# Kernel optimization log

Hardware: AMD Instinct MI355X
Metric: run time of the kernel (lower is better)

## Reference

```python
import jax, jax.numpy as jnp
from jax import lax
import numpy as np

B, T, N, F_IN, H, E, K = 8, 32, 500, 64, 128, 8000, 3
LN_EPS = 1e-5


def setup_inputs() -> dict:
    key = jax.random.key(0)
    ks = jax.random.split(key, 10)
    x = jax.random.normal(ks[0], (B, T, N, F_IN), dtype=jnp.float32)
    edge_index = jax.random.randint(ks[1], (2, E), 0, N, dtype=jnp.int64)
    edge_weight = jax.random.uniform(ks[2], (E,), dtype=jnp.float32)
    # GCNConv: linear (in->out) + bias
    W_gcn = jax.random.normal(ks[3], (F_IN, H), dtype=jnp.float32) / np.sqrt(F_IN)
    b_gcn = jnp.zeros((H,), dtype=jnp.float32)
    # Conv1d(H, H, K): weight (O, I, K)
    W_temp = jax.random.normal(ks[4], (H, H, K), dtype=jnp.float32) / np.sqrt(H * K)
    b_temp = jnp.zeros((H,), dtype=jnp.float32)
    # LayerNorm(H)
    ln_w = jnp.ones((H,), dtype=jnp.float32)
    ln_b = jnp.zeros((H,), dtype=jnp.float32)
    # residual Linear (in->out)
    W_res = jax.random.normal(ks[5], (F_IN, H), dtype=jnp.float32) / np.sqrt(F_IN)
    b_res = jnp.zeros((H,), dtype=jnp.float32)
    return {"x": x, "edge_index": edge_index, "edge_weight": edge_weight,
            "W_gcn": W_gcn, "b_gcn": b_gcn, "W_temp": W_temp, "b_temp": b_temp,
            "ln_w": ln_w, "ln_b": ln_b, "W_res": W_res, "b_res": b_res}


def reference(x, edge_index, edge_weight, W_gcn, b_gcn, W_temp, b_temp, ln_w, ln_b, W_res, b_res):
    Bv, Tv, Nv, Fv = x.shape
    Hv = W_gcn.shape[1]
    res = x @ W_res + b_res  # (B,T,N,H)

    # ---- spatial GCNConv on B*T replicated graphs (vectorized, no index offsetting) ----
    xf = x.reshape(Bv * Tv, Nv, Fv) @ W_gcn  # (BT,N,H)
    src, dst = edge_index[0], edge_index[1]
    loops = jnp.arange(Nv, dtype=edge_index.dtype)
    src2 = jnp.concatenate([src, loops])
    dst2 = jnp.concatenate([dst, loops])
    ew2 = jnp.concatenate([edge_weight, jnp.ones((Nv,), dtype=edge_weight.dtype)])
    deg = jax.ops.segment_sum(ew2, dst2, num_segments=Nv)
    dinv = jnp.where(deg > 0, deg ** -0.5, 0.0)
    norm = dinv[src2] * ew2 * dinv[dst2]  # (E+N,)
    msgs = xf[:, src2, :] * norm[None, :, None]  # (BT, E+N, H)
    agg = jax.vmap(lambda m: jax.ops.segment_sum(m, dst2, num_segments=Nv))(msgs)
    h = jax.nn.gelu(agg + b_gcn, approximate=False)  # (BT,N,H)

    # ---- temporal Conv1d over T ----
    h = h.reshape(Bv, Tv, Nv, Hv).transpose(0, 2, 3, 1).reshape(Bv * Nv, Hv, Tv)
    pad = K // 2
    h = lax.conv_general_dilated(h, W_temp, window_strides=(1,), padding=[(pad, pad)],
                                 dimension_numbers=("NCH", "OIH", "NCH"))
    h = jax.nn.gelu(h + b_temp[None, :, None], approximate=False)
    h = h.reshape(Bv, Nv, Hv, Tv).transpose(0, 3, 1, 2)  # (B,T,N,H)

    # ---- fused residual + LayerNorm over last dim ----
    y = h + res
    mu = jnp.mean(y, axis=-1, keepdims=True)
    var = jnp.mean((y - mu) ** 2, axis=-1, keepdims=True)
    return (y - mu) * lax.rsqrt(var + LN_EPS) * ln_w + ln_b
```

## Files before the change

### kernel.cpp

```cpp
#include <hip/hip_runtime.h>
#include <hip/hip_bf16.h>
#include <math.h>

#define Bv 8
#define Tv 32
#define Nv 500
#define NP 512
#define Fin 64
#define Hv 128
#define Ev 8000
#define Kv 3
#define BT (Bv*Tv)
#define ROWS (BT*Nv)
#define NCOL (BT*Fin)
#define TP (Tv+2)
#define KK (Kv*Hv)
#define LDSROW 144

typedef __attribute__((ext_vector_type(8))) short s8v;
typedef __attribute__((ext_vector_type(4))) float f4v;

__device__ __forceinline__ float gelu_exact(float v){
    float t  = v*0.70710678118654752440f;
    float ax = fabsf(t);
    float k  = __builtin_amdgcn_rcpf(fmaf(0.3275911f, ax, 1.0f));
    float p  = k*fmaf(k, fmaf(k, fmaf(k, fmaf(k, 1.061405429f, -1.453152027f),
                                      1.421413741f), -0.284496736f), 0.254829592f);
    float e  = __expf(-ax*ax);
    float er = fmaf(-p, e, 1.0f);
    er = copysignf(er, t);
    return 0.5f*v*(1.0f + er);
}
__device__ __forceinline__ short f2bs(float f){
    union { __hip_bfloat16 h; short s; } u;
    u.h = __float2bfloat16(f);
    return u.s;
}
__device__ __forceinline__ float b2f(short s){
    union { unsigned int i; float f; } u;
    u.i = ((unsigned int)(unsigned short)s) << 16;
    return u.f;
}

__global__ __launch_bounds__(1024) void k_prep0(const float* __restrict__ x,
        short* __restrict__ X2b, short* __restrict__ XT,
        float* __restrict__ Af32,
        const float* __restrict__ W, const float* __restrict__ Wg,
        const float* __restrict__ Wr,
        short* __restrict__ W2, short* __restrict__ Wgt, short* __restrict__ Wrt,
        const int* __restrict__ ei, const float* __restrict__ ew,
        float* __restrict__ dinv){
    __shared__ float sdeg[Nv];
    int bid = blockIdx.x;
    int tid = threadIdx.x;
    if (bid == 0){
        if (tid < Nv) sdeg[tid] = 1.0f;
        __syncthreads();
        for (int e = tid; e < Ev; e += 1024)
            atomicAdd(&sdeg[ei[Ev + e]], ew[e]);
        __syncthreads();
        if (tid < Nv){
            float d = sdeg[tid];
            dinv[tid] = (d > 0.f) ? rsqrtf(d) : 0.f;
        }
    } else if (bid <= 64){
        int i = (bid-1)*1024 + tid;
        ((float4*)Af32)[i] = make_float4(0.f,0.f,0.f,0.f);
    } else if (bid <= 2064){
        int gid = (bid-65)*1024 + tid;
        int row = gid >> 4, c4 = gid & 15;
        int bt = row / Nv;
        int n  = row - bt*Nv;
        float4 v = ((const float4*)x)[gid];
        short4 sv;
        sv.x = f2bs(v.x); sv.y = f2bs(v.y); sv.z = f2bs(v.z); sv.w = f2bs(v.w);
        *(short4*)(X2b + (size_t)n*NCOL + bt*64 + c4*4) = sv;
        int colb = bt*64 + c4*4;
        XT[(size_t)(colb+0)*NP + n] = sv.x;
        XT[(size_t)(colb+1)*NP + n] = sv.y;
        XT[(size_t)(colb+2)*NP + n] = sv.z;
        XT[(size_t)(colb+3)*NP + n] = sv.w;
    } else if (bid <= 2112){
        int idx = (bid-2065)*1024 + tid;
        int col = idx/3, rem = idx - col*3;
        short4 z = {0,0,0,0};
        *(short4*)(XT + (size_t)col*NP + Nv + rem*4) = z;
    } else {
        int idx = (bid-2113)*1024 + tid;
        if (idx < Hv*Hv*Kv){
            int o = idx/(Hv*Kv);
            int rem = idx - o*(Hv*Kv);
            int i = rem/Kv, k = rem - i*Kv;
            W2[o*KK + k*Hv + i] = f2bs(W[idx]);
        } else if (idx < Hv*Hv*Kv + Hv*64){
            int j = idx - Hv*Hv*Kv;
            int o = j >> 6, k = j & 63;
            Wgt[j] = f2bs(Wg[k*Hv + o]);
        } else if (idx < Hv*Hv*Kv + 2*Hv*64){
            int j = idx - Hv*Hv*Kv - Hv*64;
            int o = j >> 6, k = j & 63;
            Wrt[j] = f2bs(Wr[k*Hv + o]);
        }
    }
}

__global__ __launch_bounds__(1024) void k_prep1(const int* __restrict__ ei,
        const float* __restrict__ ew, const float* __restrict__ dinv,
        float* __restrict__ Af32){
    int e = blockIdx.x*1024 + threadIdx.x;
    if (e < Ev){
        int s = ei[e], d = ei[Ev + e];
        atomicAdd(&Af32[(size_t)d*NP + s], dinv[s]*ew[e]*dinv[d]);
    }
    if (blockIdx.x == 0 && threadIdx.x < Nv){
        float dv = dinv[threadIdx.x];
        atomicAdd(&Af32[(size_t)threadIdx.x*NP + threadIdx.x], dv*dv);
    }
}

__global__ __launch_bounds__(1024) void k_cvt(const float* __restrict__ Af32,
        short* __restrict__ Ab){
    int i = blockIdx.x*1024 + threadIdx.x;
    float4 v = ((const float4*)Af32)[i];
    short4 s;
    s.x = f2bs(v.x); s.y = f2bs(v.y); s.z = f2bs(v.z); s.w = f2bs(v.w);
    ((short4*)Ab)[i] = s;
}

__global__ __launch_bounds__(256) void k_gemm(const short* __restrict__ Ab,
        const short* __restrict__ XT, short* __restrict__ AGG2){
    int tid  = threadIdx.x;
    int w    = tid >> 6;
    int lane = tid & 63;
    int quad = lane >> 4;
    int laneo = lane & 15;
    int bid = blockIdx.x;
    int jt = bid & 127, it = bid >> 7;
    int i0 = it*128;
    int j0 = jt*128 + w*32;

    f4v acc[8][2];
    #pragma unroll
    for (int m = 0; m < 8; ++m){
        acc[m][0] = (f4v){0.f,0.f,0.f,0.f};
        acc[m][1] = (f4v){0.f,0.f,0.f,0.f};
    }
    #pragma unroll 2
    for (int ks = 0; ks < 16; ++ks){
        int k0 = ks*32 + quad*8;
        s8v bfr[2];
        #pragma unroll
        for (int nt = 0; nt < 2; ++nt)
            bfr[nt] = *(const s8v*)(XT + (size_t)(j0 + nt*16 + laneo)*NP + k0);
        #pragma unroll
        for (int m = 0; m < 8; ++m){
            s8v afr = *(const s8v*)(Ab + (size_t)(i0 + m*16 + laneo)*NP + k0);
            acc[m][0] = __builtin_amdgcn_mfma_f32_16x16x32_bf16(afr, bfr[0], acc[m][0], 0,0,0);
            acc[m][1] = __builtin_amdgcn_mfma_f32_16x16x32_bf16(afr, bfr[1], acc[m][1], 0,0,0);
        }
    }
    #pragma unroll
    for (int m = 0; m < 8; ++m){
        #pragma unroll
        for (int r = 0; r < 4; ++r){
            int row = i0 + m*16 + quad*4 + r;
            if (row < Nv){
                #pragma unroll
                for (int nt = 0; nt < 2; ++nt)
                    AGG2[(size_t)row*NCOL + j0 + nt*16 + laneo] = f2bs(acc[m][nt][r]);
            }
        }
    }
}

__global__ __launch_bounds__(256, 2) void k_mega(
        const short* __restrict__ AGG2, const short* __restrict__ X2b,
        const short* __restrict__ W2, const short* __restrict__ Wgt,
        const short* __restrict__ Wrt,
        const float* __restrict__ bg, const float* __restrict__ btm,
        const float* __restrict__ br, const float* __restrict__ lw,
        const float* __restrict__ lb, float* __restrict__ out){
    __shared__ short hs[4*TP*LDSROW];
    __shared__ float red[Tv][4][2];
    int tid  = threadIdx.x;
    int w    = tid >> 6;
    int lane = tid & 63;
    int quad = lane >> 4;
    int laneo = lane & 15;
    int bid = blockIdx.x;
    int b  = bid / 125;
    int n0 = (bid - b*125) * 4;
    int o_base = w*32;

    float bgv[2], bbv[2], brv[2], lwv[2], lbv[2];
    #pragma unroll
    for (int nt = 0; nt < 2; ++nt){
        int o = o_base + nt*16 + laneo;
        bgv[nt] = bg[o]; bbv[nt] = btm[o]; brv[nt] = br[o];
        lwv[nt] = lw[o]; lbv[nt] = lb[o];
    }

    s8v bwg[2][2];
    #pragma unroll
    for (int nt = 0; nt < 2; ++nt){
        const short* wp = Wgt + (o_base + nt*16 + laneo)*64 + quad*8;
        bwg[nt][0] = *(const s8v*)wp;
        bwg[nt][1] = *(const s8v*)(wp + 32);
    }

    if (tid < 128){
        int node = tid >> 5, rem = tid & 31;
        int tp = (rem >> 4)*(TP-1), c8 = rem & 15;
        s8v z = {0,0,0,0,0,0,0,0};
        *(s8v*)&hs[node*(TP*LDSROW) + tp*LDSROW + c8*8] = z;
    }

    for (int g = 0; g < 4; ++g){
        int n = n0 + g;
        const short* ap = AGG2 + ((size_t)n*BT + b*Tv)*64;
        #pragma unroll
        for (int m = 0; m < 2; ++m){
            const short* arp = ap + (m*16 + laneo)*64 + quad*8;
            s8v a0 = *(const s8v*)arp;
            s8v a1 = *(const s8v*)(arp + 32);
            f4v h0 = {0.f,0.f,0.f,0.f}, h1 = {0.f,0.f,0.f,0.f};
            h0 = __builtin_amdgcn_mfma_f32_16x16x32_bf16(a0, bwg[0][0], h0, 0,0,0);
            h0 = __builtin_amdgcn_mfma_f32_16x16x32_bf16(a1, bwg[0][1], h0, 0,0,0);
            h1 = __builtin_amdgcn_mfma_f32_16x16x32_bf16(a0, bwg[1][0], h1, 0,0,0);
            h1 = __builtin_amdgcn_mfma_f32_16x16x32_bf16(a1, bwg[1][1], h1, 0,0,0);
            #pragma unroll
            for (int r = 0; r < 4; ++r){
                int tp = m*16 + quad*4 + r + 1;
                short* hrow = &hs[g*(TP*LDSROW) + tp*LDSROW];
                hrow[o_base + laneo]      = f2bs(gelu_exact(h0[r] + bgv[0]));
                hrow[o_base + 16 + laneo] = f2bs(gelu_exact(h1[r] + bgv[1]));
            }
        }
    }

    s8v breg[2][12], bwr[2][2];
    #pragma unroll
    for (int nt = 0; nt < 2; ++nt){
        int o = o_base + nt*16 + laneo;
        const short* wp = W2 + o*KK + quad*8;
        #pragma unroll
        for (int s = 0; s < 12; ++s)
            breg[nt][s] = *(const s8v*)(wp + s*32);
        const short* wr = Wrt + o*64 + quad*8;
        bwr[nt][0] = *(const s8v*)wr;
        bwr[nt][1] = *(const s8v*)(wr + 32);
    }
    __syncthreads();

    for (int g = 0; g < 4; ++g){
        int n = n0 + g;
        f4v acc[2][2];
        #pragma unroll
        for (int m = 0; m < 2; ++m)
            #pragma unroll
            for (int nt = 0; nt < 2; ++nt)
                acc[m][nt] = (f4v){0.f,0.f,0.f,0.f};
        #pragma unroll
        for (int m = 0; m < 2; ++m){
            #pragma unroll
            for (int s = 0; s < 12; ++s){
                int k  = s >> 2;
                int i0 = (s & 3) * 32;
                int tp = m*16 + laneo + k;
                s8v a = *(const s8v*)&hs[g*(TP*LDSROW) + tp*LDSROW + i0 + quad*8];
                acc[m][0] = __builtin_amdgcn_mfma_f32_16x16x32_bf16(a, breg[0][s], acc[m][0], 0,0,0);
                acc[m][1] = __builtin_amdgcn_mfma_f32_16x16x32_bf16(a, breg[1][s], acc[m][1], 0,0,0);
            }
        }
        f4v racc[2][2];
        #pragma unroll
        for (int m = 0; m < 2; ++m)
            #pragma unroll
            for (int nt = 0; nt < 2; ++nt)
                racc[m][nt] = (f4v){0.f,0.f,0.f,0.f};
        const short* xp = X2b + ((size_t)n*BT + b*Tv)*64;
        #pragma unroll
        for (int m = 0; m < 2; ++m){
            const short* xrp = xp + (m*16 + laneo)*64 + quad*8;
            s8v a0 = *(const s8v*)xrp;
            s8v a1 = *(const s8v*)(xrp + 32);
            racc[m][0] = __builtin_amdgcn_mfma_f32_16x16x32_bf16(a0, bwr[0][0], racc[m][0], 0,0,0);
            racc[m][0] = __builtin_amdgcn_mfma_f32_16x16x32_bf16(a1, bwr[0][1], racc[m][0], 0,0,0);
            racc[m][1] = __builtin_amdgcn_mfma_f32_16x16x32_bf16(a0, bwr[1][0], racc[m][1], 0,0,0);
            racc[m][1] = __builtin_amdgcn_mfma_f32_16x16x32_bf16(a1, bwr[1][1], racc[m][1], 0,0,0);
        }
        size_t obase = ((size_t)b*Tv*Nv + n)*Hv;
        float yv[2][2][4];
        float srow[2][4], ssrow[2][4];
        #pragma unroll
        for (int m = 0; m < 2; ++m)
            #pragma unroll
            for (int r = 0; r < 4; ++r){ srow[m][r] = 0.f; ssrow[m][r] = 0.f; }
        #pragma unroll
        for (int m = 0; m < 2; ++m){
            #pragma unroll
            for (int nt = 0; nt < 2; ++nt){
                #pragma unroll
                for (int r = 0; r < 4; ++r){
                    float gv = gelu_exact(acc[m][nt][r] + bbv[nt]);
                    float y = gv + racc[m][nt][r] + brv[nt];
                    yv[m][nt][r] = y;
                    srow[m][r] += y; ssrow[m][r] += y*y;
                }
            }
        }
        #pragma unroll
        for (int m = 0; m < 2; ++m)
            #pragma unroll
            for (int r = 0; r < 4; ++r){
                #pragma unroll
                for (int msk = 8; msk >= 1; msk >>= 1){
                    srow[m][r]  += __shfl_xor(srow[m][r],  msk, 64);
                    ssrow[m][r] += __shfl_xor(ssrow[m][r], msk, 64);
                }
            }
        if (laneo == 0){
            #pragma unroll
            for (int m = 0; m < 2; ++m)
                #pragma unroll
                for (int r = 0; r < 4; ++r){
                    int t = m*16 + quad*4 + r;
                    red[t][w][0] = srow[m][r];
                    red[t][w][1] = ssrow[m][r];
                }
        }
        __syncthreads();
        #pragma unroll
        for (int m = 0; m < 2; ++m){
            #pragma unroll
            for (int r = 0; r < 4; ++r){
                int t = m*16 + quad*4 + r;
                float s  = red[t][0][0] + red[t][1][0] + red[t][2][0] + red[t][3][0];
                float ss = red[t][0][1] + red[t][1][1] + red[t][2][1] + red[t][3][1];
                float mu = s * (1.f/128.f);
                float var = fmaxf(ss * (1.f/128.f) - mu*mu, 0.f);
                float rstd = rsqrtf(var + 1e-5f);
                #pragma unroll
                for (int nt = 0; nt < 2; ++nt){
                    int o = o_base + nt*16 + laneo;
                    out[obase + (size_t)t*Nv*Hv + o] =
                        (yv[m][nt][r] - mu)*rstd*lwv[nt] + lbv[nt];
                }
            }
        }
        __syncthreads();
    }
}

extern "C" void kernel_launch(void* const* d_in, const int* in_sizes, int n_in,
                              void* d_out, int out_size, void* d_ws, size_t ws_size,
                              hipStream_t stream){
    const float* x   = (const float*)d_in[0];
    const int*   ei  = (const int*)d_in[1];
    const float* ew  = (const float*)d_in[2];
    const float* Wg  = (const float*)d_in[3];
    const float* bg  = (const float*)d_in[4];
    const float* Wtm = (const float*)d_in[5];
    const float* btm = (const float*)d_in[6];
    const float* lw  = (const float*)d_in[7];
    const float* lb  = (const float*)d_in[8];
    const float* Wr  = (const float*)d_in[9];
    const float* br  = (const float*)d_in[10];
    float* out = (float*)d_out;

    char* ws = (char*)d_ws;
    float* dinv = (float*)(ws + 0);
    float* Af32 = (float*)(ws + 4096);
    short* Ab   = (short*)(ws + 1052672);
    short* W2   = (short*)(ws + 1576960);
    short* Wgt  = (short*)(ws + 1675264);
    short* Wrt  = (short*)(ws + 1691648);
    short* X2b  = (short*)(ws + 1708032);
    short* XT   = (short*)(ws + 18092032);
    short* AGG2 = (short*)(ws + 34869248);

    k_prep0<<<2177, 1024, 0, stream>>>(x, X2b, XT, Af32, Wtm, Wg, Wr,
                                       W2, Wgt, Wrt, ei, ew, dinv);
    k_prep1<<<8, 1024, 0, stream>>>(ei, ew, dinv, Af32);
    k_cvt  <<<64, 1024, 0, stream>>>(Af32, Ab);
    k_gemm <<<512, 256, 0, stream>>>(Ab, XT, AGG2);
    k_mega <<<(Bv*Nv)/4, 256, 0, stream>>>(AGG2, X2b, W2, Wgt, Wrt,
                                           bg, btm, br, lw, lb, out);
}
```

Measured before the change: 220.8 us.

## Transpose x via LDS tiles and drop the X2b bf16 copy

The prep kernel now builds the transposed bf16 XT buffer through a shared-memory tile transpose, so global stores are coalesced 16-byte vectors instead of scattered 2-byte writes, and it writes the zero padding inline. The separate node-major bf16 copy X2b is removed. The mega kernel instead reads fp32 x directly and converts it to bf16 in registers for the residual MFMA. This cuts a large write and its later read, at the cost of wider fp32 loads in the mega kernel.

Measured after the change: 220.9 us. About the same (+0.0%).

```diff
diff --git a/kernel.cpp b/kernel.cpp
--- a/kernel.cpp
+++ b/kernel.cpp
@@ -36,57 +36,63 @@
     u.h = __float2bfloat16(f);
     return u.s;
 }
-__device__ __forceinline__ float b2f(short s){
-    union { unsigned int i; float f; } u;
-    u.i = ((unsigned int)(unsigned short)s) << 16;
-    return u.f;
-}
-
-__global__ __launch_bounds__(1024) void k_prep0(const float* __restrict__ x,
-        short* __restrict__ X2b, short* __restrict__ XT,
-        float* __restrict__ Af32,
+
+__global__ __launch_bounds__(256) void k_t(const float* __restrict__ x,
+        short* __restrict__ XT, float* __restrict__ Af32,
         const float* __restrict__ W, const float* __restrict__ Wg,
         const float* __restrict__ Wr,
         short* __restrict__ W2, short* __restrict__ Wgt, short* __restrict__ Wrt,
         const int* __restrict__ ei, const float* __restrict__ ew,
         float* __restrict__ dinv){
-    __shared__ float sdeg[Nv];
     int bid = blockIdx.x;
     int tid = threadIdx.x;
-    if (bid == 0){
-        if (tid < Nv) sdeg[tid] = 1.0f;
+    if (bid < 2048){
+        __shared__ short t[64][72];
+        int bt = bid >> 3;
+        int n0 = (bid & 7) * 64;
+        int r   = tid >> 2;
+        int c16 = (tid & 3) * 16;
+        int n = n0 + r;
+        short sv[16];
+        if (n < Nv){
+            const float4* src = (const float4*)(x + ((size_t)bt*Nv + n)*64 + c16);
+            #pragma unroll
+            for (int j = 0; j < 4; ++j){
+                float4 v = src[j];
+                sv[j*4+0]=f2bs(v.x); sv[j*4+1]=f2bs(v.y);
+                sv[j*4+2]=f2bs(v.z); sv[j*4+3]=f2bs(v.w);
+            }
+        } else {
+            #pragma unroll
+            for (int j = 0; j < 16; ++j) sv[j] = 0;
+        }
+        #pragma unroll
+        for (int j = 0; j < 16; ++j) t[r][c16+j] = sv[j];
         __syncthreads();
-        for (int e = tid; e < Ev; e += 1024)
+        int cc  = tid >> 2;
+        int nn0 = (tid & 3) * 16;
+        short ov[16];
+        #pragma unroll
+        for (int j = 0; j < 16; ++j) ov[j] = t[nn0+j][cc];
+        short* dst = XT + (size_t)(bt*64 + cc)*NP + n0 + nn0;
+        *(s8v*)dst       = *(s8v*)&ov[0];
+        *(s8v*)(dst + 8) = *(s8v*)&ov[8];
+    } else if (bid == 2048){
+        __shared__ float sdeg[Nv];
+        for (int i = tid; i < Nv; i += 256) sdeg[i] = 1.0f;
+        __syncthreads();
+        for (int e = tid; e < Ev; e += 256)
             atomicAdd(&sdeg[ei[Ev + e]], ew[e]);
         __syncthreads();
-        if (tid < Nv){
-            float d = sdeg[tid];
-            dinv[tid] = (d > 0.f) ? rsqrtf(d) : 0.f;
-        }
-    } else if (bid <= 64){
-        int i = (bid-1)*1024 + tid;
+        for (int i = tid; i < Nv; i += 256){
+            float d = sdeg[i];
+            dinv[i] = (d > 0.f) ? rsqrtf(d) : 0.f;
+        }
+    } else if (bid <= 2304){
+        int i = (bid-2049)*256 + tid;
         ((float4*)Af32)[i] = make_float4(0.f,0.f,0.f,0.f);
-    } else if (bid <= 2064){
-        int gid = (bid-65)*1024 + tid;
-        int row = gid >> 4, c4 = gid & 15;
-        int bt = row / Nv;
-        int n  = row - bt*Nv;
-        float4 v = ((const float4*)x)[gid];
-        short4 sv;
-        sv.x = f2bs(v.x); sv.y = f2bs(v.y); sv.z = f2bs(v.z); sv.w = f2bs(v.w);
-        *(short4*)(X2b + (size_t)n*NCOL + bt*64 + c4*4) = sv;
-        int colb = bt*64 + c4*4;
-        XT[(size_t)(colb+0)*NP + n] = sv.x;
-        XT[(size_t)(colb+1)*NP + n] = sv.y;
-        XT[(size_t)(colb+2)*NP + n] = sv.z;
-        XT[(size_t)(colb+3)*NP + n] = sv.w;
-    } else if (bid <= 2112){
-        int idx = (bid-2065)*1024 + tid;
-        int col = idx/3, rem = idx - col*3;
-        short4 z = {0,0,0,0};
-        *(short4*)(XT + (size_t)col*NP + Nv + rem*4) = z;
     } else {
-        int idx = (bid-2113)*1024 + tid;
+        int idx = (bid-2305)*256 + tid;
         if (idx < Hv*Hv*Kv){
             int o = idx/(Hv*Kv);
             int rem = idx - o*(Hv*Kv);
@@ -104,7 +110,7 @@
     }
 }
 
-__global__ __launch_bounds__(1024) void k_prep1(const int* __restrict__ ei,
+__global__ __launch_bounds__(1024) void k_scat(const int* __restrict__ ei,
         const float* __restrict__ ew, const float* __restrict__ dinv,
         float* __restrict__ Af32){
     int e = blockIdx.x*1024 + threadIdx.x;
@@ -174,7 +180,7 @@
 }
 
 __global__ __launch_bounds__(256, 2) void k_mega(
-        const short* __restrict__ AGG2, const short* __restrict__ X2b,
+        const short* __restrict__ AGG2, const float* __restrict__ x,
         const short* __restrict__ W2, const short* __restrict__ Wgt,
         const short* __restrict__ Wrt,
         const float* __restrict__ bg, const float* __restrict__ btm,
@@ -278,12 +284,18 @@
             #pragma unroll
             for (int nt = 0; nt < 2; ++nt)
                 racc[m][nt] = (f4v){0.f,0.f,0.f,0.f};
-        const short* xp = X2b + ((size_t)n*BT + b*Tv)*64;
         #pragma unroll
         for (int m = 0; m < 2; ++m){
-            const short* xrp = xp + (m*16 + laneo)*64 + quad*8;
-            s8v a0 = *(const s8v*)xrp;
-            s8v a1 = *(const s8v*)(xrp + 32);
+            const float* xr = x + (((size_t)(b*Tv + m*16 + laneo))*Nv + n)*64 + quad*8;
+            float4 f0 = *(const float4*)xr;
+            float4 f1 = *(const float4*)(xr + 4);
+            float4 f2 = *(const float4*)(xr + 32);
+            float4 f3 = *(const float4*)(xr + 36);
+            s8v a0, a1;
+            a0[0]=f2bs(f0.x); a0[1]=f2bs(f0.y); a0[2]=f2bs(f0.z); a0[3]=f2bs(f0.w);
+            a0[4]=f2bs(f1.x); a0[5]=f2bs(f1.y); a0[6]=f2bs(f1.z); a0[7]=f2bs(f1.w);
+            a1[0]=f2bs(f2.x); a1[1]=f2bs(f2.y); a1[2]=f2bs(f2.z); a1[3]=f2bs(f2.w);
+            a1[4]=f2bs(f3.x); a1[5]=f2bs(f3.y); a1[6]=f2bs(f3.z); a1[7]=f2bs(f3.w);
             racc[m][0] = __builtin_amdgcn_mfma_f32_16x16x32_bf16(a0, bwr[0][0], racc[m][0], 0,0,0);
             racc[m][0] = __builtin_amdgcn_mfma_f32_16x16x32_bf16(a1, bwr[0][1], racc[m][0], 0,0,0);
             racc[m][1] = __builtin_amdgcn_mfma_f32_16x16x32_bf16(a0, bwr[1][0], racc[m][1], 0,0,0);
@@ -375,15 +387,14 @@
     short* W2   = (short*)(ws + 1576960);
     short* Wgt  = (short*)(ws + 1675264);
     short* Wrt  = (short*)(ws + 1691648);
-    short* X2b  = (short*)(ws + 1708032);
-    short* XT   = (short*)(ws + 18092032);
-    short* AGG2 = (short*)(ws + 34869248);
-
-    k_prep0<<<2177, 1024, 0, stream>>>(x, X2b, XT, Af32, Wtm, Wg, Wr,
-                                       W2, Wgt, Wrt, ei, ew, dinv);
-    k_prep1<<<8, 1024, 0, stream>>>(ei, ew, dinv, Af32);
-    k_cvt  <<<64, 1024, 0, stream>>>(Af32, Ab);
-    k_gemm <<<512, 256, 0, stream>>>(Ab, XT, AGG2);
-    k_mega <<<(Bv*Nv)/4, 256, 0, stream>>>(AGG2, X2b, W2, Wgt, Wrt,
-                                           bg, btm, br, lw, lb, out);
-}
+    short* XT   = (short*)(ws + 1708032);
+    short* AGG2 = (short*)(ws + 18485248);
+
+    k_t   <<<2561, 256, 0, stream>>>(x, XT, Af32, Wtm, Wg, Wr,
+                                     W2, Wgt, Wrt, ei, ew, dinv);
+    k_scat<<<8, 1024, 0, stream>>>(ei, ew, dinv, Af32);
+    k_cvt <<<64, 1024, 0, stream>>>(Af32, Ab);
+    k_gemm<<<512, 256, 0, stream>>>(Ab, XT, AGG2);
+    k_mega<<<(Bv*Nv)/4, 256, 0, stream>>>(AGG2, x, W2, Wgt, Wrt,
+                                          bg, btm, br, lw, lb, out);
+}
```
